# Optimization experiments

Hardware: AMD Instinct MI355X
Metric: run time of the kernel (lower is better)

## Reference

```python
import jax, jax.numpy as jnp
import numpy as np


def setup_inputs() -> dict:
    key = jax.random.key(0)
    ks = jax.random.split(key, 12)
    B, S, H, V, T = 64, 32, 1024, 32000, 32
    s = 1.0 / np.sqrt(H)
    return {
        "encoder_outputs": jax.random.normal(ks[0], (B, S, H), jnp.float32),
        "encoder_hidden": jax.random.normal(ks[1], (1, B, H), jnp.float32),
        "input_mask": jnp.ones((B, S), dtype=bool),
        "target_tensor": jax.random.randint(ks[2], (B, T), 0, V),
        "SOS_token": 0,
        "max_len": T,
        "emb": jax.random.normal(ks[3], (V, H), jnp.float32),
        "W_ih": jax.random.uniform(ks[4], (3 * H, H), jnp.float32, -s, s),
        "W_hh": jax.random.uniform(ks[5], (3 * H, H), jnp.float32, -s, s),
        "b_ih": jax.random.uniform(ks[6], (3 * H,), jnp.float32, -s, s),
        "b_hh": jax.random.uniform(ks[7], (3 * H,), jnp.float32, -s, s),
        "out_W": jax.random.uniform(ks[8], (V, H), jnp.float32, -s, s),
        "out_b": jax.random.uniform(ks[9], (V,), jnp.float32, -s, s),
    }


def reference(encoder_outputs, encoder_hidden, input_mask, target_tensor,
              SOS_token, max_len, emb, W_ih, W_hh, b_ih, b_hh, out_W, out_b):
    B = encoder_outputs.shape[0]
    # Teacher forcing: input at step 0 is SOS, then target[:, i-1]
    tokens = jnp.concatenate(
        [jnp.full((B, 1), SOS_token, dtype=target_tensor.dtype),
         target_tensor[:, :max_len - 1]], axis=1)          # [B, T]
    # Embedding lookup + relu + input-side gate GEMM are step-independent: batch them
    x = jax.nn.relu(emb[tokens])                           # [B, T, H]
    gi = jnp.einsum('bth,gh->tbg', x, W_ih) + b_ih          # [T, B, 3H]

    def step(h, gi_t):
        gh = h @ W_hh.T + b_hh                             # [B, 3H]
        i_r, i_z, i_n = jnp.split(gi_t, 3, axis=-1)
        h_r, h_z, h_n = jnp.split(gh, 3, axis=-1)
        r = jax.nn.sigmoid(i_r + h_r)
        z = jax.nn.sigmoid(i_z + h_z)
        n = jnp.tanh(i_n + r * h_n)
        h_new = (1.0 - z) * n + z * h
        return h_new, h_new

    h0 = encoder_hidden[0]                                 # [B, H]
    h_final, hs = jax.lax.scan(step, h0, gi)               # hs: [T, B, H]
    logits = jnp.einsum('tbh,vh->btv', hs, out_W) + out_b   # [B, T, V]
    log_probs = jax.nn.log_softmax(logits, axis=-1)
    return log_probs, h_final[None]
```

## Files before the change

### kernel.cpp

```cpp
#include <hip/hip_runtime.h>
#include <hip/hip_bf16.h>
#include <math.h>

#define B_ 64
#define T_ 32
#define H_ 1024
#define V_ 32000
#define M_ (B_ * T_)
#define GRUB 64

typedef __attribute__((ext_vector_type(8))) short short8;
typedef __attribute__((ext_vector_type(4))) float f32x4;

__device__ __forceinline__ unsigned short f2bf(float f) {
  unsigned u = __float_as_uint(f);
  u = (u + 0x7FFFu + ((u >> 16) & 1u)) >> 16;
  return (unsigned short)u;
}

__device__ __forceinline__ void async16(const void* g, void* l) {
  __builtin_amdgcn_global_load_lds(
      (const __attribute__((address_space(1))) unsigned int*)g,
      (__attribute__((address_space(3))) unsigned int*)l, 16, 0, 0);
}

__global__ void k_convert(const float* __restrict__ src, short* __restrict__ dst, int n8) {
  int i = blockIdx.x * blockDim.x + threadIdx.x;
  if (i >= n8) return;
  const f32x4* s = (const f32x4*)src + (size_t)i * 2;
  f32x4 a = s[0], b = s[1];
  short8 o;
  o[0] = (short)f2bf(a[0]); o[1] = (short)f2bf(a[1]);
  o[2] = (short)f2bf(a[2]); o[3] = (short)f2bf(a[3]);
  o[4] = (short)f2bf(b[0]); o[5] = (short)f2bf(b[1]);
  o[6] = (short)f2bf(b[2]); o[7] = (short)f2bf(b[3]);
  *((short8*)dst + i) = o;
}

__global__ void k_embed(const float* __restrict__ emb, const int* __restrict__ tgt,
                        const int* __restrict__ sos, const float* __restrict__ ehid,
                        short* __restrict__ xb, short* __restrict__ hb) {
  int m = blockIdx.x, tid = threadIdx.x;
  if (m < M_) {
    int t = m >> 6, b = m & 63;
    int token = (t == 0) ? sos[0] : tgt[b * T_ + (t - 1)];
    const f32x4* s = (const f32x4*)(emb + (size_t)token * H_) + tid * 2;
    f32x4 a = s[0], c = s[1];
    short8 o;
    #pragma unroll
    for (int j = 0; j < 4; ++j) { float v = a[j] > 0.f ? a[j] : 0.f; o[j] = (short)f2bf(v); }
    #pragma unroll
    for (int j = 0; j < 4; ++j) { float v = c[j] > 0.f ? c[j] : 0.f; o[4 + j] = (short)f2bf(v); }
    *((short8*)(xb + (size_t)m * H_) + tid) = o;
  } else {
    int b = m - M_;
    const f32x4* s = (const f32x4*)(ehid + (size_t)b * H_) + tid * 2;
    f32x4 a = s[0], c = s[1];
    short8 o;
    #pragma unroll
    for (int j = 0; j < 4; ++j) o[j] = (short)f2bf(a[j]);
    #pragma unroll
    for (int j = 0; j < 4; ++j) o[4 + j] = (short)f2bf(c[j]);
    *((short8*)(hb + (size_t)b * H_) + tid) = o;
  }
}

__global__ __launch_bounds__(256, 2)
void k_gemm(const short* __restrict__ A, const short* __restrict__ Bm,
            const float* __restrict__ bias, float* __restrict__ C,
            float* __restrict__ sumexp, int N, int do_exp) {
  __shared__ short As[128 * 64];
  __shared__ short Bs[128 * 64];
  const int tid = threadIdx.x;
  const int bm = blockIdx.x, bn = blockIdx.y;
  const int w = tid >> 6, l = tid & 63;
  const int wm = (w >> 1) * 64, wn = (w & 1) * 64;
  f32x4 acc[4][4] = {};
  const short* Ab = A + (size_t)(bm * 128) * 1024;
  const short* Bb = Bm + (size_t)(bn * 128) * 1024;

  for (int kt = 0; kt < 1024; kt += 64) {
    #pragma unroll
    for (int i = 0; i < 4; ++i) {
      int g = i * 256 + tid, r = g >> 3, cp = g & 7, c = cp ^ (r & 7);
      async16(Ab + r * 1024 + kt + c * 8, &As[g * 8]);
    }
    #pragma unroll
    for (int i = 0; i < 4; ++i) {
      int g = i * 256 + tid, r = g >> 3, cp = g & 7, c = cp ^ (r & 7);
      async16(Bb + r * 1024 + kt + c * 8, &Bs[g * 8]);
    }
    __syncthreads();
    #pragma unroll
    for (int ks = 0; ks < 2; ++ks) {
      short8 af[4], bf[4];
      #pragma unroll
      for (int mi = 0; mi < 4; ++mi) {
        int row = wm + mi * 16 + (l & 15);
        int cp = (ks * 4 + (l >> 4)) ^ (row & 7);
        af[mi] = *(const short8*)&As[row * 64 + cp * 8];
      }
      #pragma unroll
      for (int ni = 0; ni < 4; ++ni) {
        int row = wn + ni * 16 + (l & 15);
        int cp = (ks * 4 + (l >> 4)) ^ (row & 7);
        bf[ni] = *(const short8*)&Bs[row * 64 + cp * 8];
      }
      #pragma unroll
      for (int mi = 0; mi < 4; ++mi)
        #pragma unroll
        for (int ni = 0; ni < 4; ++ni)
          acc[mi][ni] = __builtin_amdgcn_mfma_f32_16x16x32_bf16(af[mi], bf[ni], acc[mi][ni], 0, 0, 0);
    }
    __syncthreads();
  }

  const int row0 = bm * 128 + wm + (l >> 4) * 4;
  const int col0 = bn * 128 + wn + (l & 15);
  if (!do_exp) {
    #pragma unroll
    for (int mi = 0; mi < 4; ++mi)
      #pragma unroll
      for (int ni = 0; ni < 4; ++ni) {
        int col = col0 + ni * 16;
        float bv = bias[col];
        #pragma unroll
        for (int rg = 0; rg < 4; ++rg)
          C[(size_t)(row0 + mi * 16 + rg) * N + col] = acc[mi][ni][rg] + bv;
      }
  } else {
    #pragma unroll
    for (int mi = 0; mi < 4; ++mi) {
      float rs[4] = {0.f, 0.f, 0.f, 0.f};
      #pragma unroll
      for (int ni = 0; ni < 4; ++ni) {
        int col = col0 + ni * 16;
        float bv = bias[col];
        #pragma unroll
        for (int rg = 0; rg < 4; ++rg) {
          float v = acc[mi][ni][rg] + bv;
          C[(size_t)(row0 + mi * 16 + rg) * N + col] = v;
          rs[rg] += __expf(v);
        }
      }
      #pragma unroll
      for (int rg = 0; rg < 4; ++rg) {
        float v = rs[rg];
        #pragma unroll
        for (int off = 1; off < 16; off <<= 1) v += __shfl_xor(v, off, 64);
        if ((l & 15) == 0) atomicAdd(&sumexp[row0 + mi * 16 + rg], v);
      }
    }
  }
}

__device__ __forceinline__ void stageA(const short* __restrict__ hin, int kt,
                                       short* buf, int tid) {
  #pragma unroll
  for (int i = 0; i < 4; ++i) {
    int g = i * 256 + tid;
    int sub = g >> 9, gg = g & 511;
    int r = gg >> 3, cp = gg & 7, c = cp ^ (r & 7);
    async16(hin + (size_t)r * 1024 + kt * 128 + sub * 64 + c * 8, &buf[g * 8]);
  }
}

__global__ __launch_bounds__(256, 1)
void k_gru_persist(const short* __restrict__ Whh, const float* __restrict__ bhh,
                   const float* __restrict__ gi, const float* __restrict__ ehid,
                   short* __restrict__ hb0, short* __restrict__ hb1,
                   short* __restrict__ hs, float* __restrict__ hfin,
                   unsigned* __restrict__ barcnt) {
  __shared__ short Wlds[16 * 48 * 64];
  __shared__ short As[2][2 * 64 * 64];
  const int tid = threadIdx.x;
  const int bg = blockIdx.x;
  const int j0 = bg * 16;
  const int w = tid >> 6, l = tid & 63;

  #pragma unroll
  for (int i = 0; i < 24; ++i) {
    int idx = i * 256 + tid;
    int tile = idx / 384, rem = idx % 384;
    int r = rem >> 3, cp = rem & 7, c = cp ^ (r & 7);
    int gate = r >> 4, jr = r & 15;
    async16(Whh + ((size_t)(gate * 1024 + j0 + jr)) * 1024 + tile * 64 + c * 8,
            &Wlds[idx * 8]);
  }

  const int jj = j0 + (l & 15);
  const int b0 = w * 16 + (l >> 4) * 4;
  float hreg[4];
  #pragma unroll
  for (int rg = 0; rg < 4; ++rg) hreg[rg] = ehid[(size_t)(b0 + rg) * H_ + jj];
  const float bh_r = bhh[jj], bh_z = bhh[1024 + jj], bh_n = bhh[2048 + jj];

  for (int t = 0; t < T_; ++t) {
    const short* hin = (t & 1) ? hb1 : hb0;
    short* hout      = (t & 1) ? hb0 : hb1;
    stageA(hin, 0, As[0], tid);
    f32x4 acc[3] = {};
    for (int kt = 0; kt < 8; ++kt) {
      __syncthreads();
      if (kt < 7) stageA(hin, kt + 1, As[(kt + 1) & 1], tid);
      const short* buf = As[kt & 1];
      #pragma unroll
      for (int sub = 0; sub < 2; ++sub) {
        int kt64 = kt * 2 + sub;
        #pragma unroll
        for (int ks = 0; ks < 2; ++ks) {
          int arow = w * 16 + (l & 15);
          int acp = (ks * 4 + (l >> 4)) ^ (arow & 7);
          short8 af = *(const short8*)&buf[sub * 4096 + arow * 64 + acp * 8];
          #pragma unroll
          for (int ga = 0; ga < 3; ++ga) {
            int brow = ga * 16 + (l & 15);
            int bcp = (ks * 4 + (l >> 4)) ^ (brow & 7);
            short8 bfr = *(const short8*)&Wlds[kt64 * 3072 + brow * 64 + bcp * 8];
            acc[ga] = __builtin_amdgcn_mfma_f32_16x16x32_bf16(af, bfr, acc[ga], 0, 0, 0);
          }
        }
      }
    }
    #pragma unroll
    for (int rg = 0; rg < 4; ++rg) {
      const float* gir = gi + ((size_t)(t * 64) + b0 + rg) * 3072;
      float r = gir[jj] + acc[0][rg] + bh_r;
      r = 1.f / (1.f + __expf(-r));
      float z = gir[1024 + jj] + acc[1][rg] + bh_z;
      z = 1.f / (1.f + __expf(-z));
      float n = tanhf(gir[2048 + jj] + r * (acc[2][rg] + bh_n));
      float hn = (1.f - z) * n + z * hreg[rg];
      hreg[rg] = hn;
      short hbv = (short)f2bf(hn);
      hout[(size_t)(b0 + rg) * H_ + jj] = hbv;
      hs[((size_t)(b0 + rg) * T_ + t) * H_ + jj] = hbv;
    }
    if (t == T_ - 1) {
      #pragma unroll
      for (int rg = 0; rg < 4; ++rg) hfin[(size_t)(b0 + rg) * H_ + jj] = hreg[rg];
      break;
    }
    __syncthreads();
    if (tid == 0) {
      __threadfence();
      __hip_atomic_fetch_add(barcnt, 1u, __ATOMIC_RELEASE, __HIP_MEMORY_SCOPE_AGENT);
      while (__hip_atomic_load(barcnt, __ATOMIC_ACQUIRE, __HIP_MEMORY_SCOPE_AGENT)
             < (unsigned)(GRUB * (t + 1))) {}
      __threadfence();
    }
    __syncthreads();
  }
}

__global__ void k_lse(float* s) {
  int i = blockIdx.x * 256 + threadIdx.x;
  if (i < M_) s[i] = logf(s[i]);
}

__global__ void k_sub(float* __restrict__ out, const float* __restrict__ lse) {
  size_t vid = (size_t)blockIdx.x * 256 + threadIdx.x;
  int r = (int)(vid / (V_ / 4));
  float ls = lse[r];
  f32x4* p = (f32x4*)out + vid;
  f32x4 v = *p;
  v[0] -= ls; v[1] -= ls; v[2] -= ls; v[3] -= ls;
  *p = v;
}

extern "C" void kernel_launch(void* const* d_in, const int* in_sizes, int n_in,
                              void* d_out, int out_size, void* d_ws, size_t ws_size,
                              hipStream_t stream) {
  const float* ehid = (const float*)d_in[1];
  const int*   tgt  = (const int*)d_in[3];
  const int*   sos  = (const int*)d_in[4];
  const float* emb  = (const float*)d_in[6];
  const float* Wih  = (const float*)d_in[7];
  const float* Whh  = (const float*)d_in[8];
  const float* bih  = (const float*)d_in[9];
  const float* bhh  = (const float*)d_in[10];
  const float* outW = (const float*)d_in[11];
  const float* outb = (const float*)d_in[12];
  float* out = (float*)d_out;

  char* ws = (char*)d_ws;
  size_t off = 0;
  auto alloc = [&](size_t bytes) -> void* {
    void* p = ws + off;
    off = (off + bytes + 255) & ~(size_t)255;
    return p;
  };
  short* outW_b = (short*)alloc((size_t)V_ * H_ * 2);
  short* Wih_b  = (short*)alloc((size_t)3 * H_ * H_ * 2);
  short* Whh_b  = (short*)alloc((size_t)3 * H_ * H_ * 2);
  short* xb     = (short*)alloc((size_t)M_ * H_ * 2);
  float* gi     = (float*)alloc((size_t)M_ * 3 * H_ * 4);
  short* hs     = (short*)alloc((size_t)M_ * H_ * 2);
  short* hb0    = (short*)alloc((size_t)B_ * H_ * 2);
  short* hb1    = (short*)alloc((size_t)B_ * H_ * 2);
  float* sume   = (float*)alloc((size_t)M_ * 4);
  unsigned* barcnt = (unsigned*)alloc(256);

  k_convert<<<V_ * H_ / 8 / 256, 256, 0, stream>>>(outW, outW_b, V_ * H_ / 8);
  k_convert<<<3 * H_ * H_ / 8 / 256, 256, 0, stream>>>(Wih, Wih_b, 3 * H_ * H_ / 8);
  k_convert<<<3 * H_ * H_ / 8 / 256, 256, 0, stream>>>(Whh, Whh_b, 3 * H_ * H_ / 8);

  hipMemsetAsync(barcnt, 0, 4, stream);
  hipMemsetAsync(sume, 0, M_ * 4, stream);

  k_embed<<<M_ + B_, 128, 0, stream>>>(emb, tgt, sos, ehid, xb, hb0);

  dim3 g1(M_ / 128, 3 * H_ / 128);
  k_gemm<<<g1, 256, 0, stream>>>(xb, Wih_b, bih, gi, nullptr, 3 * H_, 0);

  k_gru_persist<<<GRUB, 256, 0, stream>>>(Whh_b, bhh, gi, ehid, hb0, hb1, hs,
                                          out + (size_t)B_ * T_ * V_, barcnt);

  dim3 g2(M_ / 128, V_ / 128);
  k_gemm<<<g2, 256, 0, stream>>>(hs, outW_b, outb, out, sume, V_, 1);

  k_lse<<<8, 256, 0, stream>>>(sume);
  k_sub<<<(int)((size_t)B_ * T_ * V_ / 4 / 256), 256, 0, stream>>>(out, sume);
}
```

Measured before the change: 1.049 ms.

## Load GRU hidden-state fragments directly to registers and lighten grid barrier

The persistent GRU kernel no longer double-buffers the hidden state through LDS with async copies and per-chunk __syncthreads. Each lane now loads all 32 of its A-operand short8 fragments straight from global memory into registers, and the gi gate inputs are prefetched before the MFMA loop. The grid barrier drops its explicit threadfences, spins with relaxed loads, and issues one agent-scope acquire fence after the block sync. This targets the latency of the sequential recurrence, at the cost of much higher register pressure and a subtler memory-ordering argument for visibility of the hidden state across blocks.

```diff
diff --git a/kernel.cpp b/kernel.cpp
--- a/kernel.cpp
+++ b/kernel.cpp
@@ -154,17 +154,6 @@
   }
 }
 
-__device__ __forceinline__ void stageA(const short* __restrict__ hin, int kt,
-                                       short* buf, int tid) {
-  #pragma unroll
-  for (int i = 0; i < 4; ++i) {
-    int g = i * 256 + tid;
-    int sub = g >> 9, gg = g & 511;
-    int r = gg >> 3, cp = gg & 7, c = cp ^ (r & 7);
-    async16(hin + (size_t)r * 1024 + kt * 128 + sub * 64 + c * 8, &buf[g * 8]);
-  }
-}
-
 __global__ __launch_bounds__(256, 1)
 void k_gru_persist(const short* __restrict__ Whh, const float* __restrict__ bhh,
                    const float* __restrict__ gi, const float* __restrict__ ehid,
@@ -172,7 +161,6 @@
                    short* __restrict__ hs, float* __restrict__ hfin,
                    unsigned* __restrict__ barcnt) {
   __shared__ short Wlds[16 * 48 * 64];
-  __shared__ short As[2][2 * 64 * 64];
   const int tid = threadIdx.x;
   const int bg = blockIdx.x;
   const int j0 = bg * 16;
@@ -195,41 +183,50 @@
   for (int rg = 0; rg < 4; ++rg) hreg[rg] = ehid[(size_t)(b0 + rg) * H_ + jj];
   const float bh_r = bhh[jj], bh_z = bhh[1024 + jj], bh_n = bhh[2048 + jj];
 
+  const int arow = w * 16 + (l & 15);
+  const int acol = (l >> 4) * 8;
+
+  __syncthreads();
+
   for (int t = 0; t < T_; ++t) {
     const short* hin = (t & 1) ? hb1 : hb0;
     short* hout      = (t & 1) ? hb0 : hb1;
-    stageA(hin, 0, As[0], tid);
-    f32x4 acc[3] = {};
-    for (int kt = 0; kt < 8; ++kt) {
-      __syncthreads();
-      if (kt < 7) stageA(hin, kt + 1, As[(kt + 1) & 1], tid);
-      const short* buf = As[kt & 1];
-      #pragma unroll
-      for (int sub = 0; sub < 2; ++sub) {
-        int kt64 = kt * 2 + sub;
-        #pragma unroll
-        for (int ks = 0; ks < 2; ++ks) {
-          int arow = w * 16 + (l & 15);
-          int acp = (ks * 4 + (l >> 4)) ^ (arow & 7);
-          short8 af = *(const short8*)&buf[sub * 4096 + arow * 64 + acp * 8];
-          #pragma unroll
-          for (int ga = 0; ga < 3; ++ga) {
-            int brow = ga * 16 + (l & 15);
-            int bcp = (ks * 4 + (l >> 4)) ^ (brow & 7);
-            short8 bfr = *(const short8*)&Wlds[kt64 * 3072 + brow * 64 + bcp * 8];
-            acc[ga] = __builtin_amdgcn_mfma_f32_16x16x32_bf16(af, bfr, acc[ga], 0, 0, 0);
-          }
-        }
-      }
-    }
+
+    float gr[4], gz[4], gn[4];
     #pragma unroll
     for (int rg = 0; rg < 4; ++rg) {
       const float* gir = gi + ((size_t)(t * 64) + b0 + rg) * 3072;
-      float r = gir[jj] + acc[0][rg] + bh_r;
+      gr[rg] = gir[jj];
+      gz[rg] = gir[1024 + jj];
+      gn[rg] = gir[2048 + jj];
+    }
+
+    const short* hrow = hin + (size_t)arow * H_ + acol;
+    short8 hf[32];
+    #pragma unroll
+    for (int ks = 0; ks < 32; ++ks)
+      hf[ks] = *(const short8*)(hrow + ks * 32);
+
+    f32x4 acc[3] = {};
+    #pragma unroll
+    for (int ks = 0; ks < 32; ++ks) {
+      int kt64 = ks >> 1, ks2 = ks & 1;
+      #pragma unroll
+      for (int ga = 0; ga < 3; ++ga) {
+        int brow = ga * 16 + (l & 15);
+        int bcp = (ks2 * 4 + (l >> 4)) ^ (brow & 7);
+        short8 bfr = *(const short8*)&Wlds[kt64 * 3072 + brow * 64 + bcp * 8];
+        acc[ga] = __builtin_amdgcn_mfma_f32_16x16x32_bf16(hf[ks], bfr, acc[ga], 0, 0, 0);
+      }
+    }
+
+    #pragma unroll
+    for (int rg = 0; rg < 4; ++rg) {
+      float r = gr[rg] + acc[0][rg] + bh_r;
       r = 1.f / (1.f + __expf(-r));
-      float z = gir[1024 + jj] + acc[1][rg] + bh_z;
+      float z = gz[rg] + acc[1][rg] + bh_z;
       z = 1.f / (1.f + __expf(-z));
-      float n = tanhf(gir[2048 + jj] + r * (acc[2][rg] + bh_n));
+      float n = tanhf(gn[rg] + r * (acc[2][rg] + bh_n));
       float hn = (1.f - z) * n + z * hreg[rg];
       hreg[rg] = hn;
       short hbv = (short)f2bf(hn);
@@ -241,15 +238,16 @@
       for (int rg = 0; rg < 4; ++rg) hfin[(size_t)(b0 + rg) * H_ + jj] = hreg[rg];
       break;
     }
+
     __syncthreads();
     if (tid == 0) {
-      __threadfence();
       __hip_atomic_fetch_add(barcnt, 1u, __ATOMIC_RELEASE, __HIP_MEMORY_SCOPE_AGENT);
-      while (__hip_atomic_load(barcnt, __ATOMIC_ACQUIRE, __HIP_MEMORY_SCOPE_AGENT)
-             < (unsigned)(GRUB * (t + 1))) {}
-      __threadfence();
+      unsigned target = (unsigned)(GRUB * (t + 1));
+      while (__hip_atomic_load(barcnt, __ATOMIC_RELAXED, __HIP_MEMORY_SCOPE_AGENT)
+             < target) {}
     }
     __syncthreads();
+    __builtin_amdgcn_fence(__ATOMIC_ACQUIRE, "agent");
   }
 }
 
```

Result: no change. 1.035 ms (-1.3%).
